# Kernel tuning notes

Measured on AMD Instinct MI355X. Metric: run time of the kernel, lower is better.

The kernel has to match this reference:

```python
import jax, jax.numpy as jnp
import numpy as np

TEMP = 10.0  # softmax_ called with N=10.0 in reduce_func

def qmul(a, b):
    # Hamilton product, rows are (w, x, y, z)
    aw, ax, ay, az = a[..., 0], a[..., 1], a[..., 2], a[..., 3]
    bw, bx, by, bz = b[..., 0], b[..., 1], b[..., 2], b[..., 3]
    return jnp.stack([
        aw * bw - ax * bx - ay * by - az * bz,
        aw * bx + ax * bw + ay * bz - az * by,
        aw * by - ax * bz + ay * bw + az * bx,
        aw * bz + ax * by - ay * bx + az * bw,
    ], axis=-1)

def setup_inputs() -> dict:
    key = jax.random.key(0)
    k1, k2, k3, k4, k5, k6 = jax.random.split(key, 6)
    N, E = 100000, 3200000
    node_levels = jax.random.uniform(k1, (N,), dtype=jnp.float32)
    node_q = jax.random.normal(k2, (N, 4), dtype=jnp.float32)
    node_q = node_q / jnp.linalg.norm(node_q, axis=1, keepdims=True)
    edge_rel_q = jax.random.normal(k3, (E, 4), dtype=jnp.float32)
    edge_rel_q = edge_rel_q / jnp.linalg.norm(edge_rel_q, axis=1, keepdims=True)
    edge_w = jax.random.uniform(k4, (E,), dtype=jnp.float32)
    src = jax.random.randint(k5, (E,), 0, N, dtype=jnp.int32)
    dst = jax.random.randint(k6, (E,), 0, N, dtype=jnp.int32)
    return {"node_levels": node_levels, "node_q": node_q,
            "edge_rel_q": edge_rel_q, "edge_w": edge_w,
            "src": src, "dst": dst}

def reference(node_levels, node_q, edge_rel_q, edge_w, src, dst):
    N = node_q.shape[0]
    # per-edge message: accumulated quaternion rel_q * q_src
    accu_q = qmul(edge_rel_q, node_q[src])          # [E,4]
    l_src = node_levels[src]                        # [E]
    # softmax logits: cost = w * l (self term has w = 1)
    cost_e = TEMP * edge_w * l_src                  # [E]
    cost_self = TEMP * node_levels                  # [N]
    # segmented stable softmax over {self} U in-edges per dst node
    seg_max = jax.ops.segment_max(cost_e, dst, num_segments=N)
    m = jnp.maximum(seg_max, cost_self)             # [N]
    exp_e = jnp.exp(cost_e - m[dst])                # [E]
    exp_self = jnp.exp(cost_self - m)               # [N]
    Z = jax.ops.segment_sum(exp_e, dst, num_segments=N) + exp_self
    # weighted sums
    sum_q = jax.ops.segment_sum(exp_e[:, None] * accu_q, dst, num_segments=N) \
            + exp_self[:, None] * node_q            # [N,4]
    sum_l = jax.ops.segment_sum(exp_e * l_src, dst, num_segments=N) \
            + exp_self * node_levels                # [N]
    out_q = sum_q / Z[:, None]
    out_levels = sum_l / Z
    # F.normalize(q, p=2, dim=1) with eps=1e-12 clamp
    norm = jnp.maximum(jnp.linalg.norm(out_q, axis=1, keepdims=True), 1e-12)
    return out_q / norm, out_levels
```

## Files before the change

kernel.cpp:

```cpp
#include <hip/hip_runtime.h>
#include <hip/hip_fp16.h>

#define TEMP 10.0f
#define TPB 512
#define HTPB 256
#define NBLK 784
#define SHIFT 9
#define GSZ 512
#define BMAX 256
#define TILE 2048
#define GTPB 1024
#define GT 4096

typedef float v2f  __attribute__((ext_vector_type(2)));
typedef float vf4  __attribute__((ext_vector_type(4)));
typedef unsigned uv4 __attribute__((ext_vector_type(4)));

__device__ __forceinline__ int   nt_i (const int* p)   { return __builtin_nontemporal_load(p); }
__device__ __forceinline__ float nt_f (const float* p) { return __builtin_nontemporal_load(p); }
__device__ __forceinline__ float4 nt_f4(const float4* p) {
    vf4 v = __builtin_nontemporal_load((const vf4*)p);
    return make_float4(v.x, v.y, v.z, v.w);
}
__device__ __forceinline__ uint4 nt_u4(const uint4* p) {
    uv4 v = __builtin_nontemporal_load((const uv4*)p);
    uint4 r; r.x = v.x; r.y = v.y; r.z = v.z; r.w = v.w; return r;
}

__device__ __forceinline__ void pk_fadd(float* p, float a, float b) {
#if __has_builtin(__builtin_amdgcn_global_atomic_fadd_v2f32)
    v2f v; v.x = a; v.y = b;
    __builtin_amdgcn_global_atomic_fadd_v2f32(
        (__attribute__((address_space(1))) v2f*)p, v);
#else
    atomicAdd(p, a); atomicAdd(p + 1, b);
#endif
}

__device__ __forceinline__ void hamilton(float4 a, float4 b,
                                         float& ow, float& ox, float& oy, float& oz) {
    ow = a.x*b.x - a.y*b.y - a.z*b.z - a.w*b.w;
    ox = a.x*b.y + a.y*b.x + a.z*b.w - a.w*b.z;
    oy = a.x*b.z - a.y*b.w + a.z*b.x + a.w*b.y;
    oz = a.x*b.w + a.y*b.z - a.z*b.y + a.w*b.x;
}

__device__ __forceinline__ unsigned f2h(float x) {
    return (unsigned)__half_as_ushort(__float2half_rn(x));
}
__device__ __forceinline__ float h2f(unsigned u) {
    return __half2float(__ushort_as_half((unsigned short)(u & 0xFFFFu)));
}

__global__ void __launch_bounds__(HTPB)
hist_kernel(const int* __restrict__ dst, unsigned* __restrict__ blkhist,
            int E, int B, int span) {
    extern __shared__ unsigned h[];
    for (int i = threadIdx.x; i < B; i += blockDim.x) h[i] = 0;
    __syncthreads();
    int start = blockIdx.x * span;
    int end = start + span; if (end > E) end = E;
    for (int e = start + threadIdx.x; e < end; e += blockDim.x)
        atomicAdd(&h[((unsigned)nt_i(&dst[e])) >> SHIFT], 1u);
    __syncthreads();
    for (int i = threadIdx.x; i < B; i += blockDim.x)
        blkhist[(size_t)i * gridDim.x + blockIdx.x] = h[i];
}

__global__ void __launch_bounds__(1024)
scan_blocks_kernel(unsigned* __restrict__ blkhist, unsigned* __restrict__ totals) {
    __shared__ unsigned s[1024];
    int b = blockIdx.x, t = threadIdx.x, n = blockDim.x;
    unsigned v = blkhist[(size_t)b * n + t];
    s[t] = v; __syncthreads();
    for (int off = 1; off < n; off <<= 1) {
        unsigned add = (t >= off) ? s[t - off] : 0u;
        __syncthreads();
        s[t] += add;
        __syncthreads();
    }
    blkhist[(size_t)b * n + t] = s[t] - v;
    if (t == n - 1) totals[b] = s[t];
}

__global__ void __launch_bounds__(1024)
scan_totals_kernel(const unsigned* __restrict__ totals,
                   unsigned* __restrict__ offsets, int B) {
    __shared__ unsigned s[1024];
    int t = threadIdx.x;
    unsigned v = (t < B) ? totals[t] : 0u;
    s[t] = v; __syncthreads();
    for (int off = 1; off < 1024; off <<= 1) {
        unsigned add = (t >= off) ? s[t - off] : 0u;
        __syncthreads();
        s[t] += add;
        __syncthreads();
    }
    if (t < B) offsets[t] = s[t] - v;
    if (t == B - 1) offsets[B] = s[t];
}

__global__ void __launch_bounds__(TPB)
scatter_sort_kernel(const float* __restrict__ nl, const float4* __restrict__ nq,
                    const float4* __restrict__ erq, const float* __restrict__ ew,
                    const int* __restrict__ src, const int* __restrict__ dst,
                    const unsigned* __restrict__ blkhist,
                    const unsigned* __restrict__ offsets,
                    uint4* __restrict__ buckets,
                    int E, int B, int span) {
    __shared__ uint4    stage[TILE];
    __shared__ unsigned gcur[BMAX];
    __shared__ unsigned th[BMAX];
    __shared__ unsigned basec[BMAX];
    __shared__ unsigned curt[BMAX];

    int blk = blockIdx.x, nb = gridDim.x, tid = threadIdx.x;
    for (int b = tid; b < B; b += TPB)
        gcur[b] = offsets[b] + blkhist[(size_t)b * nb + blk];
    int start = blk * span;
    int end = start + span; if (end > E) end = E;

    for (int ts = start; ts < end; ts += TILE) {
        int tE = end - ts; if (tE > TILE) tE = TILE;
        for (int b = tid; b < B; b += TPB) th[b] = 0;
        __syncthreads();
        for (int k = tid; k < tE; k += TPB)
            atomicAdd(&th[((unsigned)dst[ts + k]) >> SHIFT], 1u);
        __syncthreads();
        if (tid < 64) {
            int lane = tid;
            unsigned vals[4];
            unsigned tot = 0;
            #pragma unroll
            for (int c = 0; c < 4; ++c) {
                int i = lane * 4 + c;
                vals[c] = (i < B) ? th[i] : 0u;
                tot += vals[c];
            }
            unsigned inc = tot;
            #pragma unroll
            for (int off = 1; off < 64; off <<= 1) {
                unsigned up = __shfl_up(inc, off);
                if (lane >= off) inc += up;
            }
            unsigned run = inc - tot;
            #pragma unroll
            for (int c = 0; c < 4; ++c) {
                int i = lane * 4 + c;
                if (i < B) { basec[i] = run; curt[i] = run; }
                run += vals[c];
            }
        }
        __syncthreads();
        for (int k = tid; k < tE; k += TPB) {
            int e = ts + k;
            int s_ = nt_i(&src[e]);
            unsigned d = (unsigned)dst[e];
            float l = nl[s_];
            float p = __expf(TEMP * nt_f(&ew[e]) * l);
            float ow, ox, oy, oz;
            hamilton(nt_f4(&erq[e]), nq[s_], ow, ox, oy, oz);
            unsigned b = d >> SHIFT;
            unsigned pos = atomicAdd(&curt[b], 1u);
            uint4 pk;
            pk.x = (d & (GSZ - 1)) | (f2h(p) << 16);
            pk.y = f2h(p * l)  | (f2h(p * ow) << 16);
            pk.z = f2h(p * ox) | (f2h(p * oy) << 16);
            pk.w = f2h(p * oz) | (b << 16);
            stage[pos] = pk;
        }
        __syncthreads();
        for (int k = tid; k < tE; k += TPB) {
            uint4 pk = stage[k];
            unsigned b = pk.w >> 16;
            buckets[gcur[b] + ((unsigned)k - basec[b])] = pk;
        }
        __syncthreads();
        for (int b = tid; b < B; b += TPB) gcur[b] += th[b];
        __syncthreads();
    }
}

__global__ void __launch_bounds__(GTPB)
gather_sort_kernel(const float* __restrict__ nl, const float4* __restrict__ nq,
                   const unsigned* __restrict__ offsets,
                   const uint4* __restrict__ buckets,
                   float4* __restrict__ out_q, float* __restrict__ out_l, int N) {
    __shared__ unsigned s0a[GT];
    __shared__ unsigned s1a[GT];
    __shared__ unsigned s2a[GT];
    __shared__ unsigned cnt[GSZ];
    __shared__ unsigned base[GSZ + 1];

    int b = blockIdx.x, tid = threadIdx.x;
    unsigned q0 = offsets[b], q1 = offsets[b + 1];
    int M = (int)(q1 - q0);

    float accZ = 0.f, accL = 0.f, accW = 0.f, accX = 0.f, accY = 0.f, accV = 0.f;

    for (int t0 = 0; t0 < M; t0 += GT) {
        int tGT = M - t0; if (tGT > GT) tGT = GT;
        for (int i = tid; i < GSZ; i += GTPB) cnt[i] = 0;
        __syncthreads();

        uint4 pk0, pk1, pk2, pk3;
        int i0 = tid, i1 = tid + GTPB, i2 = tid + 2 * GTPB, i3 = tid + 3 * GTPB;
        if (i0 < tGT) { pk0 = nt_u4(&buckets[q0 + t0 + i0]); atomicAdd(&cnt[pk0.x & (GSZ-1)], 1u); }
        if (i1 < tGT) { pk1 = nt_u4(&buckets[q0 + t0 + i1]); atomicAdd(&cnt[pk1.x & (GSZ-1)], 1u); }
        if (i2 < tGT) { pk2 = nt_u4(&buckets[q0 + t0 + i2]); atomicAdd(&cnt[pk2.x & (GSZ-1)], 1u); }
        if (i3 < tGT) { pk3 = nt_u4(&buckets[q0 + t0 + i3]); atomicAdd(&cnt[pk3.x & (GSZ-1)], 1u); }
        __syncthreads();

        if (tid < 64) {
            unsigned vals[8], tot = 0;
            #pragma unroll
            for (int c = 0; c < 8; ++c) { vals[c] = cnt[tid * 8 + c]; tot += vals[c]; }
            unsigned inc = tot;
            #pragma unroll
            for (int off = 1; off < 64; off <<= 1) {
                unsigned up = __shfl_up(inc, off);
                if (tid >= off) inc += up;
            }
            unsigned run = inc - tot;
            #pragma unroll
            for (int c = 0; c < 8; ++c) {
                base[tid * 8 + c] = run;
                cnt[tid * 8 + c]  = run;
                run += vals[c];
            }
            if (tid == 63) base[GSZ] = run;
        }
        __syncthreads();

        if (i0 < tGT) { unsigned p = atomicAdd(&cnt[pk0.x & (GSZ-1)], 1u);
                        s0a[p] = (pk0.x >> 16) | (pk0.w << 16); s1a[p] = pk0.y; s2a[p] = pk0.z; }
        if (i1 < tGT) { unsigned p = atomicAdd(&cnt[pk1.x & (GSZ-1)], 1u);
                        s0a[p] = (pk1.x >> 16) | (pk1.w << 16); s1a[p] = pk1.y; s2a[p] = pk1.z; }
        if (i2 < tGT) { unsigned p = atomicAdd(&cnt[pk2.x & (GSZ-1)], 1u);
                        s0a[p] = (pk2.x >> 16) | (pk2.w << 16); s1a[p] = pk2.y; s2a[p] = pk2.z; }
        if (i3 < tGT) { unsigned p = atomicAdd(&cnt[pk3.x & (GSZ-1)], 1u);
                        s0a[p] = (pk3.x >> 16) | (pk3.w << 16); s1a[p] = pk3.y; s2a[p] = pk3.z; }
        __syncthreads();

        if (tid < GSZ) {
            unsigned lo = base[tid], hi = base[tid + 1];
            for (unsigned p = lo; p < hi; ++p) {
                unsigned a = s0a[p], d = s1a[p], e = s2a[p];
                accZ += h2f(a);        accV += h2f(a >> 16);
                accL += h2f(d);        accW += h2f(d >> 16);
                accX += h2f(e);        accY += h2f(e >> 16);
            }
        }
        __syncthreads();
    }

    if (tid < GSZ) {
        int n = b * GSZ + tid;
        if (n < N) {
            float l  = nl[n];
            float ps = __expf(TEMP * l);
            float Z  = accZ + ps;
            float sl = accL + ps * l;
            float4 q = nq[n];
            float qw = accW + ps * q.x;
            float qx = accX + ps * q.y;
            float qy = accY + ps * q.z;
            float qz = accV + ps * q.w;
            float inv = 1.0f / Z;
            qw *= inv; qx *= inv; qy *= inv; qz *= inv;
            float norm = fmaxf(sqrtf(qw*qw + qx*qx + qy*qy + qz*qz), 1e-12f);
            float rn = 1.0f / norm;
            out_q[n] = make_float4(qw * rn, qx * rn, qy * rn, qz * rn);
            out_l[n] = sl * inv;
        }
    }
}

__global__ void __launch_bounds__(256)
scatter_kernel(const int* __restrict__ dst, int* __restrict__ cnt,
               int* __restrict__ bucket, int cap,
               const float* __restrict__ node_levels, const float4* __restrict__ node_q,
               const float4* __restrict__ edge_rel_q, const float* __restrict__ edge_w,
               const int* __restrict__ src, float* __restrict__ side, int E) {
    int e = blockIdx.x * blockDim.x + threadIdx.x;
    if (e >= E) return;
    int d = dst[e];
    int slot = atomicAdd(&cnt[d], 1);
    if (slot < cap) {
        bucket[(long long)d * cap + slot] = e;
    } else {
        int s = src[e];
        float l = node_levels[s];
        float p = __expf(TEMP * edge_w[e] * l);
        float ow, ox, oy, oz;
        hamilton(edge_rel_q[e], node_q[s], ow, ox, oy, oz);
        float* rec = side + 6 * (long long)d;
        pk_fadd(rec + 0, p,      p * l);
        pk_fadd(rec + 2, p * ow, p * ox);
        pk_fadd(rec + 4, p * oy, p * oz);
    }
}

__global__ void __launch_bounds__(256)
gather_kernel(const float* __restrict__ node_levels, const float4* __restrict__ node_q,
              const float4* __restrict__ edge_rel_q, const float* __restrict__ edge_w,
              const int* __restrict__ src, const int* __restrict__ cnt,
              const int* __restrict__ bucket, int cap, const float* __restrict__ side,
              float4* __restrict__ out_q, float* __restrict__ out_l, int N) {
    int tid  = blockIdx.x * blockDim.x + threadIdx.x;
    int wave = tid >> 6, lane = tid & 63, half = lane >> 5, sub = lane & 31;
    int n = wave * 2 + half;
    float aZ = 0.f, aL = 0.f, a0 = 0.f, a1 = 0.f, a2 = 0.f, a3 = 0.f;
    if (n < N) {
        int deg = cnt[n]; if (deg > cap) deg = cap;
        const int* bkt = bucket + (long long)n * cap;
        for (int s = sub; s < deg; s += 32) {
            int e = bkt[s];
            int sn = src[e];
            float l = node_levels[sn];
            float p = __expf(TEMP * edge_w[e] * l);
            float ow, ox, oy, oz;
            hamilton(edge_rel_q[e], node_q[sn], ow, ox, oy, oz);
            aZ += p; aL += p * l; a0 += p * ow; a1 += p * ox; a2 += p * oy; a3 += p * oz;
        }
    }
    for (int m = 16; m; m >>= 1) {
        aZ += __shfl_xor(aZ, m); aL += __shfl_xor(aL, m);
        a0 += __shfl_xor(a0, m); a1 += __shfl_xor(a1, m);
        a2 += __shfl_xor(a2, m); a3 += __shfl_xor(a3, m);
    }
    if (sub == 0 && n < N) {
        const float* rec = side + 6 * (long long)n;
        float l  = node_levels[n];
        float ps = __expf(TEMP * l);
        float Z  = aZ + rec[0] + ps;
        float sl = aL + rec[1] + ps * l;
        float4 q = node_q[n];
        float qw = a0 + rec[2] + ps * q.x;
        float qx = a1 + rec[3] + ps * q.y;
        float qy = a2 + rec[4] + ps * q.z;
        float qz = a3 + rec[5] + ps * q.w;
        float inv = 1.0f / Z;
        qw *= inv; qx *= inv; qy *= inv; qz *= inv;
        float norm = fmaxf(sqrtf(qw*qw + qx*qx + qy*qy + qz*qz), 1e-12f);
        float rn = 1.0f / norm;
        out_q[n] = make_float4(qw * rn, qx * rn, qy * rn, qz * rn);
        out_l[n] = sl * inv;
    }
}

extern "C" void kernel_launch(void* const* d_in, const int* in_sizes, int n_in,
                              void* d_out, int out_size, void* d_ws, size_t ws_size,
                              hipStream_t stream) {
    const float*  node_levels = (const float*)d_in[0];
    const float4* node_q      = (const float4*)d_in[1];
    const float4* edge_rel_q  = (const float4*)d_in[2];
    const float*  edge_w      = (const float*)d_in[3];
    const int*    src         = (const int*)d_in[4];
    const int*    dst         = (const int*)d_in[5];

    const int N = in_sizes[0];
    const int E = in_sizes[3];

    const int B = (N + GSZ - 1) / GSZ;
    const int span = (E + NBLK - 1) / NBLK;

    size_t head_elems   = (size_t)B * NBLK + B + (B + 1);
    size_t buckets_byte = (head_elems * 4 + 15) & ~(size_t)15;
    size_t need         = buckets_byte + (size_t)E * 16;

    if (need <= ws_size && B <= BMAX) {
        unsigned* blkhist = (unsigned*)d_ws;
        unsigned* totals  = blkhist + (size_t)B * NBLK;
        unsigned* offsets = totals + B;
        uint4*    buckets = (uint4*)((char*)d_ws + buckets_byte);

        hist_kernel<<<NBLK, HTPB, B * 4, stream>>>(dst, blkhist, E, B, span);
        scan_blocks_kernel<<<B, NBLK, 0, stream>>>(blkhist, totals);
        scan_totals_kernel<<<1, 1024, 0, stream>>>(totals, offsets, B);
        scatter_sort_kernel<<<NBLK, TPB, 0, stream>>>(
            node_levels, node_q, edge_rel_q, edge_w, src, dst,
            blkhist, offsets, buckets, E, B, span);
        gather_sort_kernel<<<B, GTPB, 0, stream>>>(
            node_levels, node_q, offsets, buckets,
            (float4*)d_out, (float*)d_out + 4 * (long long)N, N);
    } else {
        const int tpb = 256;
        size_t cnt_elems  = ((size_t)N + 3) & ~(size_t)3;
        size_t side_elems = 6 * (size_t)N;
        size_t head_bytes = (cnt_elems + side_elems) * 4;
        int cap = 0;
        for (int c : {128, 64}) {
            if (head_bytes + (size_t)N * c * 4 <= ws_size) { cap = c; break; }
        }
        int*   cnt    = (int*)d_ws;
        float* side   = (float*)d_ws + cnt_elems;
        int*   bucket = (int*)d_ws + cnt_elems + side_elems;
        hipMemsetAsync(d_ws, 0, head_bytes, stream);
        scatter_kernel<<<(E + tpb - 1) / tpb, tpb, 0, stream>>>(
            dst, cnt, bucket, cap, node_levels, node_q, edge_rel_q, edge_w, src, side, E);
        int waves  = (N + 1) / 2;
        int blocks = (waves * 64 + tpb - 1) / tpb;
        gather_kernel<<<blocks, tpb, 0, stream>>>(
            node_levels, node_q, edge_rel_q, edge_w, src, cnt, bucket, cap, side,
            (float4*)d_out, (float*)d_out + 4 * (long long)N, N);
    }
}
```

Measured before the change: 228.6 us.

## Replace histogram and scan passes with atomic bucket cursors and fixed-capacity buckets

Drops the separate histogram kernel and the two prefix-scan kernels. Each scatter block now reserves space per bucket directly with a global atomicAdd on a per-bucket cursor, writing into fixed-capacity bucket segments sized from the workspace, and sends any overflow to a small spill buffer that the gather kernel scans linearly. This removes one full read of dst and three kernel launches. In exchange it adds global atomics per tile and bucket, makes the order of edges within a bucket nondeterministic, and has a serial overflow scan that would be slow if spills occurred. NBLK and TILE are also retuned.

```diff
diff --git a/kernel.cpp b/kernel.cpp
--- a/kernel.cpp
+++ b/kernel.cpp
@@ -3,14 +3,15 @@
 
 #define TEMP 10.0f
 #define TPB 512
-#define HTPB 256
-#define NBLK 784
+#define NBLK 768
 #define SHIFT 9
 #define GSZ 512
 #define BMAX 256
-#define TILE 2048
+#define TILE 2112
 #define GTPB 1024
 #define GT 4096
+#define OVCAP 16384
+#define SPILL 0xFFFFFFFFu
 
 typedef float v2f  __attribute__((ext_vector_type(2)));
 typedef float vf4  __attribute__((ext_vector_type(4)));
@@ -52,71 +53,22 @@
     return __half2float(__ushort_as_half((unsigned short)(u & 0xFFFFu)));
 }
 
-__global__ void __launch_bounds__(HTPB)
-hist_kernel(const int* __restrict__ dst, unsigned* __restrict__ blkhist,
-            int E, int B, int span) {
-    extern __shared__ unsigned h[];
-    for (int i = threadIdx.x; i < B; i += blockDim.x) h[i] = 0;
-    __syncthreads();
-    int start = blockIdx.x * span;
-    int end = start + span; if (end > E) end = E;
-    for (int e = start + threadIdx.x; e < end; e += blockDim.x)
-        atomicAdd(&h[((unsigned)nt_i(&dst[e])) >> SHIFT], 1u);
-    __syncthreads();
-    for (int i = threadIdx.x; i < B; i += blockDim.x)
-        blkhist[(size_t)i * gridDim.x + blockIdx.x] = h[i];
-}
-
-__global__ void __launch_bounds__(1024)
-scan_blocks_kernel(unsigned* __restrict__ blkhist, unsigned* __restrict__ totals) {
-    __shared__ unsigned s[1024];
-    int b = blockIdx.x, t = threadIdx.x, n = blockDim.x;
-    unsigned v = blkhist[(size_t)b * n + t];
-    s[t] = v; __syncthreads();
-    for (int off = 1; off < n; off <<= 1) {
-        unsigned add = (t >= off) ? s[t - off] : 0u;
-        __syncthreads();
-        s[t] += add;
-        __syncthreads();
-    }
-    blkhist[(size_t)b * n + t] = s[t] - v;
-    if (t == n - 1) totals[b] = s[t];
-}
-
-__global__ void __launch_bounds__(1024)
-scan_totals_kernel(const unsigned* __restrict__ totals,
-                   unsigned* __restrict__ offsets, int B) {
-    __shared__ unsigned s[1024];
-    int t = threadIdx.x;
-    unsigned v = (t < B) ? totals[t] : 0u;
-    s[t] = v; __syncthreads();
-    for (int off = 1; off < 1024; off <<= 1) {
-        unsigned add = (t >= off) ? s[t - off] : 0u;
-        __syncthreads();
-        s[t] += add;
-        __syncthreads();
-    }
-    if (t < B) offsets[t] = s[t] - v;
-    if (t == B - 1) offsets[B] = s[t];
-}
-
 __global__ void __launch_bounds__(TPB)
-scatter_sort_kernel(const float* __restrict__ nl, const float4* __restrict__ nq,
-                    const float4* __restrict__ erq, const float* __restrict__ ew,
-                    const int* __restrict__ src, const int* __restrict__ dst,
-                    const unsigned* __restrict__ blkhist,
-                    const unsigned* __restrict__ offsets,
-                    uint4* __restrict__ buckets,
-                    int E, int B, int span) {
+scatter_cursor_kernel(const float* __restrict__ nl, const float4* __restrict__ nq,
+                      const float4* __restrict__ erq, const float* __restrict__ ew,
+                      const int* __restrict__ src, const int* __restrict__ dst,
+                      unsigned* __restrict__ cursors,
+                      uint4* __restrict__ ov,
+                      uint4* __restrict__ buckets,
+                      int E, int B, int span, int CAPB) {
     __shared__ uint4    stage[TILE];
-    __shared__ unsigned gcur[BMAX];
+    __shared__ unsigned gslot[TILE];
     __shared__ unsigned th[BMAX];
     __shared__ unsigned basec[BMAX];
     __shared__ unsigned curt[BMAX];
-
-    int blk = blockIdx.x, nb = gridDim.x, tid = threadIdx.x;
-    for (int b = tid; b < B; b += TPB)
-        gcur[b] = offsets[b] + blkhist[(size_t)b * nb + blk];
+    __shared__ unsigned gbase[BMAX];
+
+    int blk = blockIdx.x, tid = threadIdx.x;
     int start = blk * span;
     int end = start + span; if (end > E) end = E;
 
@@ -127,6 +79,8 @@
         for (int k = tid; k < tE; k += TPB)
             atomicAdd(&th[((unsigned)dst[ts + k]) >> SHIFT], 1u);
         __syncthreads();
+        for (int b = tid; b < B; b += TPB)
+            gbase[b] = atomicAdd(&cursors[b], th[b]);
         if (tid < 64) {
             int lane = tid;
             unsigned vals[4];
@@ -168,24 +122,31 @@
             pk.z = f2h(p * ox) | (f2h(p * oy) << 16);
             pk.w = f2h(p * oz) | (b << 16);
             stage[pos] = pk;
+            unsigned within = gbase[b] + (pos - basec[b]);
+            gslot[pos] = (within < (unsigned)CAPB)
+                       ? ((unsigned)b * (unsigned)CAPB + within) : SPILL;
         }
         __syncthreads();
         for (int k = tid; k < tE; k += TPB) {
             uint4 pk = stage[k];
-            unsigned b = pk.w >> 16;
-            buckets[gcur[b] + ((unsigned)k - basec[b])] = pk;
-        }
-        __syncthreads();
-        for (int b = tid; b < B; b += TPB) gcur[b] += th[b];
-        __syncthreads();
+            unsigned s = gslot[k];
+            if (s != SPILL) {
+                buckets[s] = pk;
+            } else {
+                unsigned i = atomicAdd(&cursors[B], 1u);
+                if (i < (unsigned)OVCAP) ov[i] = pk;
+            }
+        }
     }
 }
 
 __global__ void __launch_bounds__(GTPB)
 gather_sort_kernel(const float* __restrict__ nl, const float4* __restrict__ nq,
-                   const unsigned* __restrict__ offsets,
+                   const unsigned* __restrict__ cursors,
+                   const uint4* __restrict__ ov,
                    const uint4* __restrict__ buckets,
-                   float4* __restrict__ out_q, float* __restrict__ out_l, int N) {
+                   float4* __restrict__ out_q, float* __restrict__ out_l,
+                   int N, int B, int CAPB) {
     __shared__ unsigned s0a[GT];
     __shared__ unsigned s1a[GT];
     __shared__ unsigned s2a[GT];
@@ -193,8 +154,9 @@
     __shared__ unsigned base[GSZ + 1];
 
     int b = blockIdx.x, tid = threadIdx.x;
-    unsigned q0 = offsets[b], q1 = offsets[b + 1];
-    int M = (int)(q1 - q0);
+    unsigned total = cursors[b];
+    int M = (int)(total < (unsigned)CAPB ? total : (unsigned)CAPB);
+    const uint4* seg = buckets + (size_t)b * (size_t)CAPB;
 
     float accZ = 0.f, accL = 0.f, accW = 0.f, accX = 0.f, accY = 0.f, accV = 0.f;
 
@@ -205,10 +167,10 @@
 
         uint4 pk0, pk1, pk2, pk3;
         int i0 = tid, i1 = tid + GTPB, i2 = tid + 2 * GTPB, i3 = tid + 3 * GTPB;
-        if (i0 < tGT) { pk0 = nt_u4(&buckets[q0 + t0 + i0]); atomicAdd(&cnt[pk0.x & (GSZ-1)], 1u); }
-        if (i1 < tGT) { pk1 = nt_u4(&buckets[q0 + t0 + i1]); atomicAdd(&cnt[pk1.x & (GSZ-1)], 1u); }
-        if (i2 < tGT) { pk2 = nt_u4(&buckets[q0 + t0 + i2]); atomicAdd(&cnt[pk2.x & (GSZ-1)], 1u); }
-        if (i3 < tGT) { pk3 = nt_u4(&buckets[q0 + t0 + i3]); atomicAdd(&cnt[pk3.x & (GSZ-1)], 1u); }
+        if (i0 < tGT) { pk0 = nt_u4(&seg[t0 + i0]); atomicAdd(&cnt[pk0.x & (GSZ-1)], 1u); }
+        if (i1 < tGT) { pk1 = nt_u4(&seg[t0 + i1]); atomicAdd(&cnt[pk1.x & (GSZ-1)], 1u); }
+        if (i2 < tGT) { pk2 = nt_u4(&seg[t0 + i2]); atomicAdd(&cnt[pk2.x & (GSZ-1)], 1u); }
+        if (i3 < tGT) { pk3 = nt_u4(&seg[t0 + i3]); atomicAdd(&cnt[pk3.x & (GSZ-1)], 1u); }
         __syncthreads();
 
         if (tid < 64) {
@@ -255,6 +217,15 @@
     }
 
     if (tid < GSZ) {
+        unsigned ovc = cursors[B]; if (ovc > (unsigned)OVCAP) ovc = OVCAP;
+        for (unsigned i = 0; i < ovc; ++i) {
+            uint4 pk = ov[i];
+            if ((pk.w >> 16) == (unsigned)b && (int)(pk.x & (GSZ - 1)) == tid) {
+                accZ += h2f(pk.x >> 16); accV += h2f(pk.w);
+                accL += h2f(pk.y);       accW += h2f(pk.y >> 16);
+                accX += h2f(pk.z);       accY += h2f(pk.z >> 16);
+            }
+        }
         int n = b * GSZ + tid;
         if (n < N) {
             float l  = nl[n];
@@ -365,25 +336,32 @@
     const int B = (N + GSZ - 1) / GSZ;
     const int span = (E + NBLK - 1) / NBLK;
 
-    size_t head_elems   = (size_t)B * NBLK + B + (B + 1);
-    size_t buckets_byte = (head_elems * 4 + 15) & ~(size_t)15;
-    size_t need         = buckets_byte + (size_t)E * 16;
-
-    if (need <= ws_size && B <= BMAX) {
-        unsigned* blkhist = (unsigned*)d_ws;
-        unsigned* totals  = blkhist + (size_t)B * NBLK;
-        unsigned* offsets = totals + B;
-        uint4*    buckets = (uint4*)((char*)d_ws + buckets_byte);
-
-        hist_kernel<<<NBLK, HTPB, B * 4, stream>>>(dst, blkhist, E, B, span);
-        scan_blocks_kernel<<<B, NBLK, 0, stream>>>(blkhist, totals);
-        scan_totals_kernel<<<1, 1024, 0, stream>>>(totals, offsets, B);
-        scatter_sort_kernel<<<NBLK, TPB, 0, stream>>>(
+    size_t head  = (((size_t)(B + 1) * 4) + 15) & ~(size_t)15;
+    size_t fixed = head + (size_t)OVCAP * 16;
+
+    int CAPB = 0;
+    bool ok = false;
+    if (B >= 1 && B <= BMAX && ws_size > fixed) {
+        size_t capb = (ws_size - fixed) / ((size_t)B * 16);
+        long long mean = (E + B) / B;
+        if ((long long)capb >= mean + 2048) {
+            ok = true;
+            CAPB = (int)((capb < 0x7FFFFFFF) ? capb : 0x7FFFFFFF);
+        }
+    }
+
+    if (ok) {
+        unsigned* cursors = (unsigned*)d_ws;
+        uint4*    ov      = (uint4*)((char*)d_ws + head);
+        uint4*    buckets = ov + OVCAP;
+
+        hipMemsetAsync(d_ws, 0, (size_t)(B + 1) * 4, stream);
+        scatter_cursor_kernel<<<NBLK, TPB, 0, stream>>>(
             node_levels, node_q, edge_rel_q, edge_w, src, dst,
-            blkhist, offsets, buckets, E, B, span);
+            cursors, ov, buckets, E, B, span, CAPB);
         gather_sort_kernel<<<B, GTPB, 0, stream>>>(
-            node_levels, node_q, offsets, buckets,
-            (float4*)d_out, (float*)d_out + 4 * (long long)N, N);
+            node_levels, node_q, cursors, ov, buckets,
+            (float4*)d_out, (float*)d_out + 4 * (long long)N, N, B, CAPB);
     } else {
         const int tpb = 256;
         size_t cnt_elems  = ((size_t)N + 3) & ~(size_t)3;
```

Measured after the change: 215.2 us. 5.8% less time.
